# Kernel optimization log

Measured on AMD Instinct MI355X. Metric: run time of the kernel, lower is better.

## Reference

```python
import jax, jax.numpy as jnp
import numpy as np

D_MODEL, H, D_K, D_V = 512, 8, 64, 64
S_Q, S_KV = 2048, 2048


def setup_inputs() -> dict:
    key = jax.random.key(0)
    ks = jax.random.split(key, 11)
    sc = 0.02
    return {
        "embeddings": jax.random.normal(ks[0], (S_Q, D_MODEL), jnp.float32),
        "K": jax.random.normal(ks[1], (S_KV, D_MODEL), jnp.float32),
        "V": jax.random.normal(ks[2], (S_KV, D_MODEL), jnp.float32),
        # per-head projection weights (stacked over heads) + biases
        "Wq": jax.random.normal(ks[3], (H, D_MODEL, D_K), jnp.float32) * sc,
        "bq": jax.random.normal(ks[4], (H, D_K), jnp.float32) * sc,
        "Wk": jax.random.normal(ks[5], (H, D_MODEL, D_K), jnp.float32) * sc,
        "bk": jax.random.normal(ks[6], (H, D_K), jnp.float32) * sc,
        "Wv": jax.random.normal(ks[7], (H, D_MODEL, D_V), jnp.float32) * sc,
        "bv": jax.random.normal(ks[8], (H, D_V), jnp.float32) * sc,
        # final linear: [h*d_v -> d_model]
        "Wo": jax.random.normal(ks[9], (H * D_V, D_MODEL), jnp.float32) * sc,
        "bo": jax.random.normal(ks[10], (D_MODEL,), jnp.float32) * sc,
    }


def reference(embeddings, K, V, Wq, bq, Wk, bk, Wv, bv, Wo, bo):
    # Batched per-head projections (the original loops over h heads; math identical)
    q = jnp.einsum("sd,hdk->hsk", embeddings, Wq) + bq[:, None, :]  # [h, Sq, d_k]
    k = jnp.einsum("td,hdk->htk", K, Wk) + bk[:, None, :]           # [h, Skv, d_k]
    v = jnp.einsum("td,hdv->htv", V, Wv) + bv[:, None, :]           # [h, Skv, d_v]
    scores = jnp.einsum("hsk,htk->hst", q, k) / jnp.sqrt(jnp.asarray(D_K, q.dtype))
    attn = jax.nn.softmax(scores, axis=-1)                           # [h, Sq, Skv]
    out = jnp.einsum("hst,htv->hsv", attn, v)                        # [h, Sq, d_v]
    # torch.cat(results, dim=1): head 0's d_v columns first -> [Sq, h*d_v]
    concat = jnp.transpose(out, (1, 0, 2)).reshape(S_Q, H * D_V)
    return concat @ Wo + bo                                          # [Sq, d_model]
```

## Files before the change

kernel.cpp:

```cpp
#include <hip/hip_runtime.h>

#define SQ 2048
#define DM 512
#define NH 8
#define NSPLIT 4

typedef __bf16 bf16x8 __attribute__((ext_vector_type(8)));
typedef float f32x4 __attribute__((ext_vector_type(4)));
typedef unsigned short us8 __attribute__((ext_vector_type(8)));

__device__ __forceinline__ unsigned short f2bf(float f) {
    unsigned u = __builtin_bit_cast(unsigned, f);
    u += 0x7fffu + ((u >> 16) & 1u);
    return (unsigned short)(u >> 16);
}
__device__ __forceinline__ float bf2f(unsigned short u) {
    return __builtin_bit_cast(float, (unsigned)u << 16);
}

__global__ __launch_bounds__(256) void convert_all(
    const float* __restrict__ emb, const float* __restrict__ Kin, const float* __restrict__ Vin,
    const float* __restrict__ Wq,  const float* __restrict__ Wk,  const float* __restrict__ Wv,
    const float* __restrict__ Wo,
    unsigned short* __restrict__ xe, unsigned short* __restrict__ xk, unsigned short* __restrict__ xv,
    unsigned short* __restrict__ Wt,
    unsigned short* __restrict__ Woth, unsigned short* __restrict__ Wotl)
{
    const int b = blockIdx.x, tid = threadIdx.x;
    __shared__ float ld[64 * 68];
    float4* ld4 = reinterpret_cast<float4*>(ld);

    if (b < 1536) {
        const int m = b >> 9;
        const float* src = (m == 0) ? emb : (m == 1) ? Kin : Vin;
        unsigned short* dst = (m == 0) ? xe : (m == 1) ? xk : xv;
        const int oct = (b & 511) * 256 + tid;
        const float4* s4 = reinterpret_cast<const float4*>(src + (size_t)oct * 8);
        float4 f0 = s4[0], f1 = s4[1];
        us8 o;
        o[0] = f2bf(f0.x); o[1] = f2bf(f0.y); o[2] = f2bf(f0.z); o[3] = f2bf(f0.w);
        o[4] = f2bf(f1.x); o[5] = f2bf(f1.y); o[6] = f2bf(f1.z); o[7] = f2bf(f1.w);
        *reinterpret_cast<us8*>(dst + (size_t)oct * 8) = o;
    } else if (b < 1728) {
        const int wi = b - 1536;
        const int idx = wi >> 3;
        const int kt = wi & 7;
        const int p = idx >> 3, h = idx & 7;
        const float* src = ((p == 0) ? Wq : (p == 1) ? Wk : Wv)
                         + (size_t)h * 512 * 64 + (size_t)kt * 64 * 64;
        unsigned short* dst = Wt + (size_t)idx * 64 * 512 + kt * 64;
        const int rr = tid >> 4, c4 = tid & 15;
        #pragma unroll
        for (int it = 0; it < 4; it++) {
            int r = rr + 16 * it;
            ld4[r * 17 + c4] = reinterpret_cast<const float4*>(src + (size_t)r * 64)[c4];
        }
        __syncthreads();
        #pragma unroll
        for (int it = 0; it < 2; it++) {
            int slot = tid + it * 256;
            int n = slot >> 3, g = slot & 7;
            us8 o;
            #pragma unroll
            for (int i = 0; i < 8; i++)
                o[i] = f2bf(ld[(g * 8 + i) * 68 + n]);
            *reinterpret_cast<us8*>(dst + (size_t)n * 512 + g * 8) = o;
        }
    } else {
        const int ti = b - 1728;
        const int kt = ti >> 3, nt = ti & 7;
        const float* src = Wo + (size_t)kt * 64 * 512 + nt * 64;
        const int rr = tid >> 4, c4 = tid & 15;
        #pragma unroll
        for (int it = 0; it < 4; it++) {
            int r = rr + 16 * it;
            ld4[r * 17 + c4] = reinterpret_cast<const float4*>(src + (size_t)r * 512)[c4];
        }
        __syncthreads();
        #pragma unroll
        for (int it = 0; it < 2; it++) {
            int slot = tid + it * 256;
            int n = slot >> 3, g = slot & 7;
            us8 oh, ol;
            #pragma unroll
            for (int i = 0; i < 8; i++) {
                float v = ld[(g * 8 + i) * 68 + n];
                unsigned short hi = f2bf(v);
                oh[i] = hi;
                ol[i] = f2bf(v - bf2f(hi));
            }
            size_t doff = (size_t)(nt * 64 + n) * 512 + kt * 64 + g * 8;
            *reinterpret_cast<us8*>(Woth + doff) = oh;
            *reinterpret_cast<us8*>(Wotl + doff) = ol;
        }
    }
}

__global__ __launch_bounds__(256) void qkv_mfma(
    const unsigned short* __restrict__ xe, const unsigned short* __restrict__ xk,
    const unsigned short* __restrict__ xv, const unsigned short* __restrict__ Wt,
    const float* __restrict__ bq, const float* __restrict__ bk, const float* __restrict__ bv,
    unsigned short* __restrict__ qo, unsigned short* __restrict__ ko, unsigned short* __restrict__ vo)
{
    const int p = blockIdx.z, h = blockIdx.y, s0 = blockIdx.x * 64;
    const unsigned short* X = (p == 0) ? xe : (p == 1) ? xk : xv;
    const unsigned short* W = Wt + (size_t)(p * 8 + h) * 64 * 512;
    const float* B = ((p == 0) ? bq : (p == 1) ? bk : bv) + h * 64;

    const int tid = threadIdx.x;
    const int w = tid >> 6, lane = tid & 63, cl = lane & 15, q4 = lane >> 4;
    const int sr = tid >> 3, sg = tid & 7;

    __shared__ unsigned short As[2][64 * 72];
    __shared__ unsigned short Bs[2][64 * 72];

    #pragma unroll
    for (int it = 0; it < 2; it++) {
        int r = sr + 32 * it;
        *reinterpret_cast<float4*>(&As[0][r * 72 + sg * 8]) =
            *reinterpret_cast<const float4*>(&X[(size_t)(s0 + r) * 512 + sg * 8]);
        *reinterpret_cast<float4*>(&Bs[0][r * 72 + sg * 8]) =
            *reinterpret_cast<const float4*>(&W[(size_t)r * 512 + sg * 8]);
    }

    f32x4 acc[4] = {};

    for (int c = 0; c < 8; c++) {
        __syncthreads();
        const int buf = c & 1;
        const bool more = (c + 1 < 8);
        float4 ar[2], br[2];
        if (more) {
            #pragma unroll
            for (int it = 0; it < 2; it++) {
                int r = sr + 32 * it;
                ar[it] = *reinterpret_cast<const float4*>(
                    &X[(size_t)(s0 + r) * 512 + (c + 1) * 64 + sg * 8]);
                br[it] = *reinterpret_cast<const float4*>(
                    &W[(size_t)r * 512 + (c + 1) * 64 + sg * 8]);
            }
        }

        bf16x8 a0 = *reinterpret_cast<const bf16x8*>(&As[buf][(16 * w + cl) * 72 + q4 * 8]);
        bf16x8 a1 = *reinterpret_cast<const bf16x8*>(&As[buf][(16 * w + cl) * 72 + 32 + q4 * 8]);
        #pragma unroll
        for (int nn = 0; nn < 4; nn++) {
            bf16x8 b0 = *reinterpret_cast<const bf16x8*>(&Bs[buf][(16 * nn + cl) * 72 + q4 * 8]);
            bf16x8 b1 = *reinterpret_cast<const bf16x8*>(&Bs[buf][(16 * nn + cl) * 72 + 32 + q4 * 8]);
            acc[nn] = __builtin_amdgcn_mfma_f32_16x16x32_bf16(a0, b0, acc[nn], 0, 0, 0);
            acc[nn] = __builtin_amdgcn_mfma_f32_16x16x32_bf16(a1, b1, acc[nn], 0, 0, 0);
        }

        if (more) {
            const int nbuf = buf ^ 1;
            #pragma unroll
            for (int it = 0; it < 2; it++) {
                int r = sr + 32 * it;
                *reinterpret_cast<float4*>(&As[nbuf][r * 72 + sg * 8]) = ar[it];
                *reinterpret_cast<float4*>(&Bs[nbuf][r * 72 + sg * 8]) = br[it];
            }
        }
    }

    if (p == 0) {
        #pragma unroll
        for (int nn = 0; nn < 4; nn++) {
            int col = 16 * nn + cl;
            float bb = B[col];
            #pragma unroll
            for (int r = 0; r < 4; r++)
                qo[((size_t)h * SQ + s0 + 16 * w + q4 * 4 + r) * 64 + col] =
                    f2bf((acc[nn][r] + bb) * 0.125f);
        }
    } else if (p == 1) {
        #pragma unroll
        for (int nn = 0; nn < 4; nn++) {
            int col = 16 * nn + cl;
            float bb = B[col];
            #pragma unroll
            for (int r = 0; r < 4; r++)
                ko[((size_t)h * SQ + s0 + 16 * w + q4 * 4 + r) * 64 + col] =
                    f2bf(acc[nn][r] + bb);
        }
    } else {
        #pragma unroll
        for (int nn = 0; nn < 4; nn++) {
            int col = 16 * nn + cl;
            float bb = B[col];
            ushort4 o;
            o.x = f2bf(acc[nn][0] + bb);
            o.y = f2bf(acc[nn][1] + bb);
            o.z = f2bf(acc[nn][2] + bb);
            o.w = f2bf(acc[nn][3] + bb);
            *reinterpret_cast<ushort4*>(
                vo + ((size_t)h * 64 + col) * SQ + s0 + 16 * w + q4 * 4) = o;
        }
    }
}

#define PW 72

__global__ __launch_bounds__(256) void attn_fwd(
    const unsigned short* __restrict__ qbf,
    const unsigned short* __restrict__ kbf,
    const unsigned short* __restrict__ vbf,
    float* __restrict__ Opart,
    float* __restrict__ lpart)
{
    const int h = blockIdx.y, s0 = blockIdx.x * 64, z = blockIdx.z;
    const int tid = threadIdx.x;
    const int w = tid >> 6, lane = tid & 63, cl = lane & 15, q4 = lane >> 4;
    const int NT = SQ / 64 / NSPLIT;
    const int t0 = z * NT;

    __shared__ unsigned short Ks[2][64 * PW];
    __shared__ unsigned short Vs[2][64 * PW];
    __shared__ unsigned short Ps[4][16 * PW];

    bf16x8 aq0 = *reinterpret_cast<const bf16x8*>(
        &qbf[((size_t)h * SQ + s0 + 16 * w + cl) * 64 + q4 * 8]);
    bf16x8 aq1 = *reinterpret_cast<const bf16x8*>(
        &qbf[((size_t)h * SQ + s0 + 16 * w + cl) * 64 + 32 + q4 * 8]);

    const int sr = tid >> 3, sg = tid & 7;

    #pragma unroll
    for (int it = 0; it < 2; it++) {
        int r = sr + 32 * it;
        *reinterpret_cast<float4*>(&Ks[0][r * PW + sg * 8]) =
            *reinterpret_cast<const float4*>(&kbf[((size_t)h * SQ + t0 * 64 + r) * 64 + sg * 8]);
        *reinterpret_cast<float4*>(&Vs[0][r * PW + sg * 8]) =
            *reinterpret_cast<const float4*>(&vbf[((size_t)h * 64 + r) * SQ + t0 * 64 + sg * 8]);
    }

    f32x4 o_acc[4] = {};
    float lsum[4] = {};

    for (int tl = 0; tl < NT; tl++) {
        __syncthreads();
        const int buf = tl & 1;
        const bool more = (tl + 1 < NT);
        float4 kr[2], vr[2];
        if (more) {
            #pragma unroll
            for (int it = 0; it < 2; it++) {
                int r = sr + 32 * it;
                kr[it] = *reinterpret_cast<const float4*>(
                    &kbf[((size_t)h * SQ + (t0 + tl + 1) * 64 + r) * 64 + sg * 8]);
                vr[it] = *reinterpret_cast<const float4*>(
                    &vbf[((size_t)h * 64 + r) * SQ + (t0 + tl + 1) * 64 + sg * 8]);
            }
        }

        f32x4 s_acc[4] = {};
        #pragma unroll
        for (int nn = 0; nn < 4; nn++) {
            bf16x8 b0 = *reinterpret_cast<const bf16x8*>(&Ks[buf][(16 * nn + cl) * PW + q4 * 8]);
            bf16x8 b1 = *reinterpret_cast<const bf16x8*>(&Ks[buf][(16 * nn + cl) * PW + 32 + q4 * 8]);
            s_acc[nn] = __builtin_amdgcn_mfma_f32_16x16x32_bf16(aq0, b0, s_acc[nn], 0, 0, 0);
            s_acc[nn] = __builtin_amdgcn_mfma_f32_16x16x32_bf16(aq1, b1, s_acc[nn], 0, 0, 0);
        }

        #pragma unroll
        for (int r = 0; r < 4; r++) {
            #pragma unroll
            for (int nn = 0; nn < 4; nn++) {
                float pv = __expf(s_acc[nn][r]);
                lsum[r] += pv;
                Ps[w][(q4 * 4 + r) * PW + 16 * nn + cl] = f2bf(pv);
            }
        }
        bf16x8 ap0 = *reinterpret_cast<const bf16x8*>(&Ps[w][cl * PW + q4 * 8]);
        bf16x8 ap1 = *reinterpret_cast<const bf16x8*>(&Ps[w][cl * PW + 32 + q4 * 8]);

        #pragma unroll
        for (int nn = 0; nn < 4; nn++) {
            bf16x8 b0 = *reinterpret_cast<const bf16x8*>(&Vs[buf][(16 * nn + cl) * PW + q4 * 8]);
            bf16x8 b1 = *reinterpret_cast<const bf16x8*>(&Vs[buf][(16 * nn + cl) * PW + 32 + q4 * 8]);
            o_acc[nn] = __builtin_amdgcn_mfma_f32_16x16x32_bf16(ap0, b0, o_acc[nn], 0, 0, 0);
            o_acc[nn] = __builtin_amdgcn_mfma_f32_16x16x32_bf16(ap1, b1, o_acc[nn], 0, 0, 0);
        }

        if (more) {
            const int nbuf = buf ^ 1;
            #pragma unroll
            for (int it = 0; it < 2; it++) {
                int r = sr + 32 * it;
                *reinterpret_cast<float4*>(&Ks[nbuf][r * PW + sg * 8]) = kr[it];
                *reinterpret_cast<float4*>(&Vs[nbuf][r * PW + sg * 8]) = vr[it];
            }
        }
    }

    #pragma unroll
    for (int r = 0; r < 4; r++) {
        float v = lsum[r];
        #pragma unroll
        for (int off = 1; off < 16; off <<= 1) v += __shfl_xor(v, off);
        lsum[r] = v;
    }

    const size_t zb = (size_t)(z * NH + h);
    if (cl == 0) {
        #pragma unroll
        for (int r = 0; r < 4; r++)
            lpart[zb * SQ + s0 + 16 * w + q4 * 4 + r] = lsum[r];
    }
    #pragma unroll
    for (int nn = 0; nn < 4; nn++)
        #pragma unroll
        for (int r = 0; r < 4; r++)
            Opart[(zb * SQ + s0 + 16 * w + q4 * 4 + r) * 64 + 16 * nn + cl] = o_acc[nn][r];
}

__global__ __launch_bounds__(256) void attn_combine(
    const float* __restrict__ Opart, const float* __restrict__ lpart,
    unsigned short* __restrict__ athi, unsigned short* __restrict__ atlo)
{
    const int gid = blockIdx.x * 256 + threadIdx.x;
    const int s = gid >> 6, oct = gid & 63;
    const int col0 = oct * 8, h = col0 >> 6, dv0 = col0 & 63;

    float l = 0.f;
    #pragma unroll
    for (int z = 0; z < NSPLIT; z++)
        l += lpart[(size_t)(z * NH + h) * SQ + s];
    const float inv = 1.0f / l;

    float o[8] = {};
    #pragma unroll
    for (int z = 0; z < NSPLIT; z++) {
        const float4* base = reinterpret_cast<const float4*>(
            Opart + ((size_t)(z * NH + h) * SQ + s) * 64 + dv0);
        float4 a = base[0], bq = base[1];
        o[0] += a.x; o[1] += a.y; o[2] += a.z; o[3] += a.w;
        o[4] += bq.x; o[5] += bq.y; o[6] += bq.z; o[7] += bq.w;
    }
    us8 hi, lo;
    #pragma unroll
    for (int i = 0; i < 8; i++) {
        float v = o[i] * inv;
        unsigned short hb = f2bf(v);
        hi[i] = hb;
        lo[i] = f2bf(v - bf2f(hb));
    }
    *reinterpret_cast<us8*>(athi + (size_t)s * DM + col0) = hi;
    *reinterpret_cast<us8*>(atlo + (size_t)s * DM + col0) = lo;
}

__global__ __launch_bounds__(256) void out_proj(
    const unsigned short* __restrict__ ah, const unsigned short* __restrict__ al,
    const unsigned short* __restrict__ Wh, const unsigned short* __restrict__ Wl,
    const float* __restrict__ bo, float* __restrict__ out)
{
    const int s0 = blockIdx.x * 64, n0 = blockIdx.y * 64;
    const int tid = threadIdx.x;
    const int w = tid >> 6, lane = tid & 63, cl = lane & 15, q4 = lane >> 4;
    const int sr = tid >> 3, sg = tid & 7;

    __shared__ unsigned short Ah[2][64 * 72], Al[2][64 * 72];
    __shared__ unsigned short Bh[2][64 * 72], Bl[2][64 * 72];

    #pragma unroll
    for (int it = 0; it < 2; it++) {
        int r = sr + 32 * it;
        *reinterpret_cast<float4*>(&Ah[0][r * 72 + sg * 8]) =
            *reinterpret_cast<const float4*>(&ah[(size_t)(s0 + r) * 512 + sg * 8]);
        *reinterpret_cast<float4*>(&Al[0][r * 72 + sg * 8]) =
            *reinterpret_cast<const float4*>(&al[(size_t)(s0 + r) * 512 + sg * 8]);
        *reinterpret_cast<float4*>(&Bh[0][r * 72 + sg * 8]) =
            *reinterpret_cast<const float4*>(&Wh[(size_t)(n0 + r) * 512 + sg * 8]);
        *reinterpret_cast<float4*>(&Bl[0][r * 72 + sg * 8]) =
            *reinterpret_cast<const float4*>(&Wl[(size_t)(n0 + r) * 512 + sg * 8]);
    }

    f32x4 acc[4] = {};

    for (int c = 0; c < 8; c++) {
        __syncthreads();
        const int buf = c & 1;
        const bool more = (c + 1 < 8);
        float4 ahr[2], alr[2], bhr[2], blr[2];
        if (more) {
            #pragma unroll
            for (int it = 0; it < 2; it++) {
                int r = sr + 32 * it;
                int off = (c + 1) * 64 + sg * 8;
                ahr[it] = *reinterpret_cast<const float4*>(&ah[(size_t)(s0 + r) * 512 + off]);
                alr[it] = *reinterpret_cast<const float4*>(&al[(size_t)(s0 + r) * 512 + off]);
                bhr[it] = *reinterpret_cast<const float4*>(&Wh[(size_t)(n0 + r) * 512 + off]);
                blr[it] = *reinterpret_cast<const float4*>(&Wl[(size_t)(n0 + r) * 512 + off]);
            }
        }

        bf16x8 ah0 = *reinterpret_cast<const bf16x8*>(&Ah[buf][(16 * w + cl) * 72 + q4 * 8]);
        bf16x8 ah1 = *reinterpret_cast<const bf16x8*>(&Ah[buf][(16 * w + cl) * 72 + 32 + q4 * 8]);
        bf16x8 al0 = *reinterpret_cast<const bf16x8*>(&Al[buf][(16 * w + cl) * 72 + q4 * 8]);
        bf16x8 al1 = *reinterpret_cast<const bf16x8*>(&Al[buf][(16 * w + cl) * 72 + 32 + q4 * 8]);
        #pragma unroll
        for (int nn = 0; nn < 4; nn++) {
            bf16x8 bh0 = *reinterpret_cast<const bf16x8*>(&Bh[buf][(16 * nn + cl) * 72 + q4 * 8]);
            bf16x8 bh1 = *reinterpret_cast<const bf16x8*>(&Bh[buf][(16 * nn + cl) * 72 + 32 + q4 * 8]);
            bf16x8 bl0 = *reinterpret_cast<const bf16x8*>(&Bl[buf][(16 * nn + cl) * 72 + q4 * 8]);
            bf16x8 bl1 = *reinterpret_cast<const bf16x8*>(&Bl[buf][(16 * nn + cl) * 72 + 32 + q4 * 8]);
            acc[nn] = __builtin_amdgcn_mfma_f32_16x16x32_bf16(ah0, bh0, acc[nn], 0, 0, 0);
            acc[nn] = __builtin_amdgcn_mfma_f32_16x16x32_bf16(ah1, bh1, acc[nn], 0, 0, 0);
            acc[nn] = __builtin_amdgcn_mfma_f32_16x16x32_bf16(ah0, bl0, acc[nn], 0, 0, 0);
            acc[nn] = __builtin_amdgcn_mfma_f32_16x16x32_bf16(ah1, bl1, acc[nn], 0, 0, 0);
            acc[nn] = __builtin_amdgcn_mfma_f32_16x16x32_bf16(al0, bh0, acc[nn], 0, 0, 0);
            acc[nn] = __builtin_amdgcn_mfma_f32_16x16x32_bf16(al1, bh1, acc[nn], 0, 0, 0);
        }

        if (more) {
            const int nbuf = buf ^ 1;
            #pragma unroll
            for (int it = 0; it < 2; it++) {
                int r = sr + 32 * it;
                *reinterpret_cast<float4*>(&Ah[nbuf][r * 72 + sg * 8]) = ahr[it];
                *reinterpret_cast<float4*>(&Al[nbuf][r * 72 + sg * 8]) = alr[it];
                *reinterpret_cast<float4*>(&Bh[nbuf][r * 72 + sg * 8]) = bhr[it];
                *reinterpret_cast<float4*>(&Bl[nbuf][r * 72 + sg * 8]) = blr[it];
            }
        }
    }

    #pragma unroll
    for (int nn = 0; nn < 4; nn++) {
        int col = n0 + 16 * nn + cl;
        float bb = bo[col];
        #pragma unroll
        for (int r = 0; r < 4; r++)
            out[(size_t)(s0 + 16 * w + q4 * 4 + r) * DM + col] = acc[nn][r] + bb;
    }
}

extern "C" void kernel_launch(void* const* d_in, const int* in_sizes, int n_in,
                              void* d_out, int out_size, void* d_ws, size_t ws_size,
                              hipStream_t stream) {
    const float* emb = (const float*)d_in[0];
    const float* Kin = (const float*)d_in[1];
    const float* Vin = (const float*)d_in[2];
    const float* Wq  = (const float*)d_in[3];
    const float* bq  = (const float*)d_in[4];
    const float* Wk  = (const float*)d_in[5];
    const float* bk  = (const float*)d_in[6];
    const float* Wv  = (const float*)d_in[7];
    const float* bv  = (const float*)d_in[8];
    const float* Wo  = (const float*)d_in[9];
    const float* bo  = (const float*)d_in[10];
    float* out = (float*)d_out;

    unsigned short* p = (unsigned short*)d_ws;
    unsigned short* xe   = p; p += (size_t)SQ * DM;
    unsigned short* xk   = p; p += (size_t)SQ * DM;
    unsigned short* xv   = p; p += (size_t)SQ * DM;
    unsigned short* Wt   = p; p += (size_t)24 * 64 * 512;
    unsigned short* Woth = p; p += (size_t)512 * 512;
    unsigned short* Wotl = p; p += (size_t)512 * 512;
    unsigned short* qbf  = p; p += (size_t)NH * SQ * 64;
    unsigned short* kbf  = p; p += (size_t)NH * SQ * 64;
    unsigned short* vbf  = p; p += (size_t)NH * SQ * 64;
    unsigned short* athi = p; p += (size_t)SQ * DM;
    unsigned short* atlo = p; p += (size_t)SQ * DM;
    float* Opart = (float*)p;
    float* lpart = Opart + (size_t)NSPLIT * NH * SQ * 64;

    convert_all<<<1792, 256, 0, stream>>>(emb, Kin, Vin, Wq, Wk, Wv, Wo,
                                          xe, xk, xv, Wt, Woth, Wotl);
    qkv_mfma<<<dim3(32, 8, 3), 256, 0, stream>>>(xe, xk, xv, Wt, bq, bk, bv,
                                                 qbf, kbf, vbf);
    attn_fwd<<<dim3(32, 8, NSPLIT), 256, 0, stream>>>(qbf, kbf, vbf, Opart, lpart);
    attn_combine<<<512, 256, 0, stream>>>(Opart, lpart, athi, atlo);
    out_proj<<<dim3(32, 8), 256, 0, stream>>>(athi, atlo, Woth, Wotl, bo, out);
}
```

Measured before the change: 127.6 us.

## Keep P in registers via transposed QK^T MFMA and permuted V layout

Result: faster. 121.2 us (-5.0%).

```diff
diff --git a/kernel.cpp b/kernel.cpp
--- a/kernel.cpp
+++ b/kernel.cpp
@@ -8,6 +8,7 @@
 typedef __bf16 bf16x8 __attribute__((ext_vector_type(8)));
 typedef float f32x4 __attribute__((ext_vector_type(4)));
 typedef unsigned short us8 __attribute__((ext_vector_type(8)));
+typedef unsigned short us4 __attribute__((ext_vector_type(4)));
 
 __device__ __forceinline__ unsigned short f2bf(float f) {
     unsigned u = __builtin_bit_cast(unsigned, f);
@@ -163,6 +164,7 @@
     }
 
     if (p == 0) {
+        const float QSCALE = 0.125f * 1.4426950408889634f;
         #pragma unroll
         for (int nn = 0; nn < 4; nn++) {
             int col = 16 * nn + cl;
@@ -170,7 +172,7 @@
             #pragma unroll
             for (int r = 0; r < 4; r++)
                 qo[((size_t)h * SQ + s0 + 16 * w + q4 * 4 + r) * 64 + col] =
-                    f2bf((acc[nn][r] + bb) * 0.125f);
+                    f2bf((acc[nn][r] + bb) * QSCALE);
         }
     } else if (p == 1) {
         #pragma unroll
@@ -200,7 +202,7 @@
 
 #define PW 72
 
-__global__ __launch_bounds__(256) void attn_fwd(
+__global__ __launch_bounds__(256, 4) void attn_fwd(
     const unsigned short* __restrict__ qbf,
     const unsigned short* __restrict__ kbf,
     const unsigned short* __restrict__ vbf,
@@ -215,7 +217,6 @@
 
     __shared__ unsigned short Ks[2][64 * PW];
     __shared__ unsigned short Vs[2][64 * PW];
-    __shared__ unsigned short Ps[4][16 * PW];
 
     bf16x8 aq0 = *reinterpret_cast<const bf16x8*>(
         &qbf[((size_t)h * SQ + s0 + 16 * w + cl) * 64 + q4 * 8]);
@@ -223,31 +224,36 @@
         &qbf[((size_t)h * SQ + s0 + 16 * w + cl) * 64 + 32 + q4 * 8]);
 
     const int sr = tid >> 3, sg = tid & 7;
+    const int kapA = 32 * (sg >> 2) + 16 * (sg & 1) + 4 * ((sg >> 1) & 1);
 
     #pragma unroll
     for (int it = 0; it < 2; it++) {
         int r = sr + 32 * it;
         *reinterpret_cast<float4*>(&Ks[0][r * PW + sg * 8]) =
             *reinterpret_cast<const float4*>(&kbf[((size_t)h * SQ + t0 * 64 + r) * 64 + sg * 8]);
-        *reinterpret_cast<float4*>(&Vs[0][r * PW + sg * 8]) =
-            *reinterpret_cast<const float4*>(&vbf[((size_t)h * 64 + r) * SQ + t0 * 64 + sg * 8]);
+        us8 vv = *reinterpret_cast<const us8*>(&vbf[((size_t)h * 64 + r) * SQ + t0 * 64 + sg * 8]);
+        *reinterpret_cast<us4*>(&Vs[0][r * PW + kapA]) =
+            __builtin_shufflevector(vv, vv, 0, 1, 2, 3);
+        *reinterpret_cast<us4*>(&Vs[0][r * PW + kapA + 8]) =
+            __builtin_shufflevector(vv, vv, 4, 5, 6, 7);
     }
 
     f32x4 o_acc[4] = {};
-    float lsum[4] = {};
+    float lsum = 0.f;
 
     for (int tl = 0; tl < NT; tl++) {
         __syncthreads();
         const int buf = tl & 1;
         const bool more = (tl + 1 < NT);
-        float4 kr[2], vr[2];
+        float4 kr[2];
+        us8 vr[2];
         if (more) {
             #pragma unroll
             for (int it = 0; it < 2; it++) {
                 int r = sr + 32 * it;
                 kr[it] = *reinterpret_cast<const float4*>(
                     &kbf[((size_t)h * SQ + (t0 + tl + 1) * 64 + r) * 64 + sg * 8]);
-                vr[it] = *reinterpret_cast<const float4*>(
+                vr[it] = *reinterpret_cast<const us8*>(
                     &vbf[((size_t)h * 64 + r) * SQ + (t0 + tl + 1) * 64 + sg * 8]);
             }
         }
@@ -255,23 +261,23 @@
         f32x4 s_acc[4] = {};
         #pragma unroll
         for (int nn = 0; nn < 4; nn++) {
-            bf16x8 b0 = *reinterpret_cast<const bf16x8*>(&Ks[buf][(16 * nn + cl) * PW + q4 * 8]);
-            bf16x8 b1 = *reinterpret_cast<const bf16x8*>(&Ks[buf][(16 * nn + cl) * PW + 32 + q4 * 8]);
-            s_acc[nn] = __builtin_amdgcn_mfma_f32_16x16x32_bf16(aq0, b0, s_acc[nn], 0, 0, 0);
-            s_acc[nn] = __builtin_amdgcn_mfma_f32_16x16x32_bf16(aq1, b1, s_acc[nn], 0, 0, 0);
-        }
-
-        #pragma unroll
-        for (int r = 0; r < 4; r++) {
-            #pragma unroll
-            for (int nn = 0; nn < 4; nn++) {
-                float pv = __expf(s_acc[nn][r]);
-                lsum[r] += pv;
-                Ps[w][(q4 * 4 + r) * PW + 16 * nn + cl] = f2bf(pv);
-            }
-        }
-        bf16x8 ap0 = *reinterpret_cast<const bf16x8*>(&Ps[w][cl * PW + q4 * 8]);
-        bf16x8 ap1 = *reinterpret_cast<const bf16x8*>(&Ps[w][cl * PW + 32 + q4 * 8]);
+            bf16x8 k0 = *reinterpret_cast<const bf16x8*>(&Ks[buf][(16 * nn + cl) * PW + q4 * 8]);
+            bf16x8 k1 = *reinterpret_cast<const bf16x8*>(&Ks[buf][(16 * nn + cl) * PW + 32 + q4 * 8]);
+            s_acc[nn] = __builtin_amdgcn_mfma_f32_16x16x32_bf16(k0, aq0, s_acc[nn], 0, 0, 0);
+            s_acc[nn] = __builtin_amdgcn_mfma_f32_16x16x32_bf16(k1, aq1, s_acc[nn], 0, 0, 0);
+        }
+
+        bf16x8 ap0, ap1;
+        #pragma unroll
+        for (int nn = 0; nn < 4; nn++) {
+            #pragma unroll
+            for (int r = 0; r < 4; r++) {
+                float pv = __builtin_amdgcn_exp2f(s_acc[nn][r]);
+                lsum += pv;
+                if (nn < 2) ap0[nn * 4 + r] = (__bf16)pv;
+                else        ap1[(nn - 2) * 4 + r] = (__bf16)pv;
+            }
+        }
 
         #pragma unroll
         for (int nn = 0; nn < 4; nn++) {
@@ -287,25 +293,21 @@
             for (int it = 0; it < 2; it++) {
                 int r = sr + 32 * it;
                 *reinterpret_cast<float4*>(&Ks[nbuf][r * PW + sg * 8]) = kr[it];
-                *reinterpret_cast<float4*>(&Vs[nbuf][r * PW + sg * 8]) = vr[it];
-            }
-        }
-    }
-
-    #pragma unroll
-    for (int r = 0; r < 4; r++) {
-        float v = lsum[r];
-        #pragma unroll
-        for (int off = 1; off < 16; off <<= 1) v += __shfl_xor(v, off);
-        lsum[r] = v;
-    }
+                *reinterpret_cast<us4*>(&Vs[nbuf][r * PW + kapA]) =
+                    __builtin_shufflevector(vr[it], vr[it], 0, 1, 2, 3);
+                *reinterpret_cast<us4*>(&Vs[nbuf][r * PW + kapA + 8]) =
+                    __builtin_shufflevector(vr[it], vr[it], 4, 5, 6, 7);
+            }
+        }
+    }
+
+    lsum += __shfl_xor(lsum, 16);
+    lsum += __shfl_xor(lsum, 32);
 
     const size_t zb = (size_t)(z * NH + h);
-    if (cl == 0) {
-        #pragma unroll
-        for (int r = 0; r < 4; r++)
-            lpart[zb * SQ + s0 + 16 * w + q4 * 4 + r] = lsum[r];
-    }
+    if (q4 == 0)
+        lpart[zb * SQ + s0 + 16 * w + cl] = lsum;
+
     #pragma unroll
     for (int nn = 0; nn < 4; nn++)
         #pragma unroll
```
